# Kernel tuning notes

Hardware: AMD Instinct MI355X
Metric: run time of the kernel (lower is better)

## Reference

```python
import jax, jax.numpy as jnp
import numpy as np

# Static configuration (from init_kwargs)
SPLIT_SEC = (128, 320, 320)   # (n_nucl_species..., n_up, n_dn)
N = sum(SPLIT_SEC)            # 768 particles
N_NUCL = sum(SPLIT_SEC[:-2])  # 128
N_DN = SPLIT_SEC[-1]          # 320
SINGLE = 256
PAIR = 64
D_FEAT = SINGLE + len(SPLIT_SEC) * PAIR + len(SPLIT_SEC) * SINGLE  # 1216
SQRT2 = 1.4142135623730951
GELU_RESCALE = 1.7128586      # fvmc rescaled-gelu constant (unit output variance)

_SPLIT_IDX = np.cumsum(SPLIT_SEC)[:-1]

def _pair_type():
    pt = np.zeros((N, N), np.int32)
    sn, se = slice(0, N_NUCL), slice(N_NUCL, N)
    su = slice(N_NUCL, N_NUCL + SPLIT_SEC[-2])
    sd = slice(N_NUCL + SPLIT_SEC[-2], N)
    pt[sn, se] = pt[se, sn] = 1
    pt[su, su] = pt[sd, sd] = 2
    pt[su, sd] = pt[sd, su] = 3
    return pt

PAIR_TYPE = _pair_type()  # static int mask, values in {0,1,2,3}

def actv(x):
    # parse_activation('gelu', rescale=True)
    return jax.nn.gelu(x) * GELU_RESCALE

def residual(x, y):
    # adaptive_residual with rescale=True (shapes always match here)
    return (x + y) / SQRT2

def aggregate_features(h1, h2):
    # per-section mean of h1 over particles -> (n_sec, d1), tiled to (N, n_sec, d1)
    h1_mean = jnp.stack([s.mean(axis=0) for s in jnp.split(h1, _SPLIT_IDX, axis=0)], axis=0)
    h1_mean = jnp.tile(h1_mean[None], (N, 1, 1))
    # per-section mean of h2 over axis 1 -> (N, n_sec, d2)
    h2_mean = jnp.stack([s.mean(axis=1) for s in jnp.split(h2, _SPLIT_IDX, axis=1)], axis=-2)
    # spin symmetry: swap the last two (up/dn) mean channels for the dn rows
    h1_sw = jnp.stack([h1_mean[-N_DN:, -1], h1_mean[-N_DN:, -2]], axis=1)
    h1_mean = h1_mean.at[-N_DN:, -2:].set(h1_sw)
    h2_sw = jnp.stack([h2_mean[-N_DN:, -1], h2_mean[-N_DN:, -2]], axis=1)
    h2_mean = h2_mean.at[-N_DN:, -2:].set(h2_sw)
    return jnp.concatenate([h1, h2_mean.reshape(N, -1), h1_mean.reshape(N, -1)], axis=-1)

def setup_inputs() -> dict:
    key = jax.random.key(0)
    ks = jax.random.split(key, 5)
    sc = lambda fan_in: 1.0 / np.sqrt(fan_in)  # lecun-normal-ish scale
    return {
        "h1": jax.random.normal(ks[0], (N, SINGLE), jnp.float32),
        "h2": jax.random.normal(ks[1], (N, N, PAIR), jnp.float32),
        "W1n": jax.random.normal(ks[2], (D_FEAT, SINGLE), jnp.float32) * sc(D_FEAT),
        "b1n": jnp.zeros((SINGLE,), jnp.float32),
        "W1e": jax.random.normal(ks[3], (D_FEAT, SINGLE), jnp.float32) * sc(D_FEAT),
        "b1e": jnp.zeros((SINGLE,), jnp.float32),
        "W2": jax.random.normal(ks[4], (4, PAIR, PAIR), jnp.float32) * sc(PAIR),
        "b2": jnp.zeros((4, PAIR), jnp.float32),
    }

def reference(h1, h2, W1n, b1n, W1e, b1e, W2, b2):
    feats = aggregate_features(h1, h2)  # (N, D_FEAT)
    # h1 update: separate Dense for nuclei vs electrons
    h1_new = jnp.concatenate([
        feats[:N_NUCL] @ W1n + b1n,
        feats[N_NUCL:] @ W1e + b1e,
    ], axis=0)
    h1_out = residual(h1, actv(h1_new))
    # h2 update: per pair-type Dense, masked scatter back (4 static types)
    pt = jnp.asarray(PAIR_TYPE)
    h2_new = jnp.zeros((N, N, PAIR), h2.dtype)
    for p in range(4):
        mask = (pt == p)[..., None]
        h2_new = h2_new + mask * (jnp.einsum('nmd,de->nme', h2, W2[p]) + b2[p])
    h2_out = residual(h2, actv(h2_new))
    return h1_out, h2_out
```

## Files before the change

kernel.cpp:

```cpp
#include <hip/hip_runtime.h>


#define H1OUT_ELEMS (768 * 256)

typedef short short8 __attribute__((ext_vector_type(8)));
typedef float f32x4 __attribute__((ext_vector_type(4)));

__device__ __forceinline__ unsigned short f2bf(float f) {
    unsigned u = __builtin_bit_cast(unsigned, f);
    unsigned r = u + 0x7fffu + ((u >> 16) & 1u);
    return (unsigned short)(r >> 16);
}

__device__ __forceinline__ float bf2f(unsigned short v) {
    unsigned u = ((unsigned)v) << 16;
    return __builtin_bit_cast(float, u);
}

__device__ __forceinline__ float gelu_res(float x, float hv) {
    float x2 = x * x;
    float z = x * fmaf(-0.1029432196f, x2, -2.3025850930f);
    float e = __builtin_amdgcn_exp2f(z);
    float r = __builtin_amdgcn_rcpf(1.f + e);
    return fmaf(x * r, 1.2111740f, hv * 0.70710678f);
}

__global__ __launch_bounds__(256) void k_h2pre(
    const float* __restrict__ h2, const float* __restrict__ W2,
    const float* __restrict__ b2, const float* __restrict__ h1,
    const float* __restrict__ W1n, const float* __restrict__ W1e,
    float* __restrict__ out2, float* __restrict__ part2,
    float* __restrict__ part1, unsigned short* __restrict__ WT) {
    __shared__ union SM {
        unsigned short ot[4][16][76];
        unsigned short BT[64][72];
        float tile2[64][33];
    } sm;
    __shared__ float red[4][4][64];

    int b = blockIdx.x;
    const int t = threadIdx.x;

    if (b < 12) {
        float s = 0.f;
        #pragma unroll 8
        for (int r = 0; r < 64; ++r) s += h1[(size_t)(b * 64 + r) * 256 + t];
        part1[b * 256 + t] = s;
        return;
    }
    if (b < 316) {
        int idx = b - 12;
        int mtx = idx / 152;
        int r2  = idx % 152;
        int k0 = (r2 >> 3) * 64, e0 = (r2 & 7) * 32;
        const float* W = mtx ? W1e : W1n;
        #pragma unroll
        for (int i = 0; i < 8; ++i) {
            int j = i * 256 + t;
            int kr = j >> 5, ec = j & 31;
            sm.tile2[kr][ec] = W[(size_t)(k0 + kr) * 256 + e0 + ec];
        }
        __syncthreads();
        int er = t >> 3, k8 = (t & 7) * 8;
        short8 o;
        #pragma unroll
        for (int j = 0; j < 8; ++j) o[j] = (short)f2bf(sm.tile2[k8 + j][er]);
        *reinterpret_cast<short8*>(
            &WT[((size_t)mtx * 256 + e0 + er) * 1216 + k0 + k8]) = o;
        return;
    }

    b -= 316;
    const int ct = b % 12;
    const int n  = b / 12;
    const int m0 = ct * 64;

    const int rs = (n < 128) ? 0 : ((n < 448) ? 1 : 2);
    const int cs = (ct < 2) ? 0 : ((ct < 7) ? 1 : 2);
    int p;
    if (rs == 0)      p = (cs == 0) ? 0 : 1;
    else if (rs == 1) p = (cs == 0) ? 1 : ((cs == 1) ? 2 : 3);
    else              p = (cs == 0) ? 1 : ((cs == 1) ? 3 : 2);

    const float* src = h2 + ((size_t)n * 768 + m0) * 64;
    const int lane = t & 63;
    const int w = t >> 6;
    const int lr = lane & 15, lk = lane >> 4;
    const int r0 = w * 16;

    const float* wrow = W2 + p * 4096 + lane * 64 + w * 16;
    float4 wv4[4];
    #pragma unroll
    for (int i = 0; i < 4; ++i)
        wv4[i] = *reinterpret_cast<const float4*>(wrow + i * 4);

    const float* hbase = src + r0 * 64;
    f32x4 hv[4];
    #pragma unroll
    for (int i = 0; i < 4; ++i)
        hv[i] = *reinterpret_cast<const f32x4*>(hbase + i * 256 + lane * 4);

    const float* arow = src + (r0 + lr) * 64 + lk * 8;
    float4 af[2][2];
    #pragma unroll
    for (int kh = 0; kh < 2; ++kh) {
        af[kh][0] = *reinterpret_cast<const float4*>(arow + kh * 32);
        af[kh][1] = *reinterpret_cast<const float4*>(arow + kh * 32 + 4);
    }

    #pragma unroll
    for (int i = 0; i < 4; ++i) {
        unsigned short v0 = f2bf(wv4[i].x);
        unsigned short v1 = f2bf(wv4[i].y);
        unsigned short v2 = f2bf(wv4[i].z);
        unsigned short v3 = f2bf(wv4[i].w);
        sm.BT[w * 16 + i * 4 + 0][lane] = v0;
        sm.BT[w * 16 + i * 4 + 1][lane] = v1;
        sm.BT[w * 16 + i * 4 + 2][lane] = v2;
        sm.BT[w * 16 + i * 4 + 3][lane] = v3;
    }

    {
        f32x4 s;
        s[0] = hv[0][0] + hv[1][0] + hv[2][0] + hv[3][0];
        s[1] = hv[0][1] + hv[1][1] + hv[2][1] + hv[3][1];
        s[2] = hv[0][2] + hv[1][2] + hv[2][2] + hv[3][2];
        s[3] = hv[0][3] + hv[1][3] + hv[2][3] + hv[3][3];
        *reinterpret_cast<f32x4*>(&red[w][lane >> 4][(lane & 15) * 4]) = s;
    }

    asm volatile("s_waitcnt lgkmcnt(0)" ::: "memory");
    __builtin_amdgcn_s_barrier();
    asm volatile("" ::: "memory");

    if (t < 64) {
        float s = 0.f;
        #pragma unroll
        for (int q = 0; q < 16; ++q) s += red[q >> 2][q & 3][t];
        part2[((size_t)n * 12 + ct) * 64 + t] = s;
    }

    short8 bF[4][2];
    #pragma unroll
    for (int fe = 0; fe < 4; ++fe)
        #pragma unroll
        for (int kh = 0; kh < 2; ++kh)
            bF[fe][kh] = *reinterpret_cast<const short8*>(
                &sm.BT[fe * 16 + lr][kh * 32 + lk * 8]);

    short8 aF[2];
    #pragma unroll
    for (int kh = 0; kh < 2; ++kh) {
        short8 o;
        o[0] = (short)f2bf(af[kh][0].x);
        o[1] = (short)f2bf(af[kh][0].y);
        o[2] = (short)f2bf(af[kh][0].z);
        o[3] = (short)f2bf(af[kh][0].w);
        o[4] = (short)f2bf(af[kh][1].x);
        o[5] = (short)f2bf(af[kh][1].y);
        o[6] = (short)f2bf(af[kh][1].z);
        o[7] = (short)f2bf(af[kh][1].w);
        aF[kh] = o;
    }

    asm volatile("s_waitcnt lgkmcnt(0)" ::: "memory");
    __builtin_amdgcn_s_barrier();
    asm volatile("" ::: "memory");

    #pragma unroll
    for (int fe = 0; fe < 4; ++fe) {
        f32x4 acc = {};
        acc = __builtin_amdgcn_mfma_f32_16x16x32_bf16(aF[0], bF[fe][0], acc, 0, 0, 0);
        acc = __builtin_amdgcn_mfma_f32_16x16x32_bf16(aF[1], bF[fe][1], acc, 0, 0, 0);
        float bias = b2[p * 64 + fe * 16 + lr];
        #pragma unroll
        for (int r = 0; r < 4; ++r)
            sm.ot[w][lk * 4 + r][fe * 16 + lr] = f2bf(acc[r] + bias);
    }

    float* dst = out2 + ((size_t)n * 768 + m0 + r0) * 64;
    #pragma unroll
    for (int i = 0; i < 4; ++i) {
        int row = i * 4 + (lane >> 4), col = (lane & 15) * 4;
        ushort4 xb = *reinterpret_cast<const ushort4*>(&sm.ot[w][row][col]);
        f32x4 o;
        o[0] = gelu_res(bf2f(xb.x), hv[i][0]);
        o[1] = gelu_res(bf2f(xb.y), hv[i][1]);
        o[2] = gelu_res(bf2f(xb.z), hv[i][2]);
        o[3] = gelu_res(bf2f(xb.w), hv[i][3]);
        __builtin_nontemporal_store(
            o, reinterpret_cast<f32x4*>(dst + i * 256 + lane * 4));
    }
}

__global__ __launch_bounds__(256) void k_h1f(
    const float* __restrict__ h1, const unsigned short* __restrict__ WT,
    const float* __restrict__ part2, const float* __restrict__ part1,
    const float* __restrict__ b1n, const float* __restrict__ b1e,
    float* __restrict__ out1) {
    __shared__ unsigned short FL[16][1224];

    const int n0 = blockIdx.x * 16;
    const int half = blockIdx.y;
    const int t = threadIdx.x;
    const bool dn = (n0 >= 448);
    const bool nucl = (n0 < 128);

    #pragma unroll
    for (int i = 0; i < 16; ++i) {
        int idx = i * 256 + t;
        int r = idx >> 8, c = idx & 255;
        FL[r][c] = f2bf(h1[(size_t)(n0 + r) * 256 + c]);
    }
    #pragma unroll
    for (int i = 0; i < 12; ++i) {
        int idx = i * 256 + t;
        int r = idx / 192, c = idx % 192;
        int sec = c >> 6, d = c & 63;
        int s2 = (dn && sec >= 1) ? (3 - sec) : sec;
        const float* pr = part2 + (size_t)(n0 + r) * 768;
        float s;
        if (s2 == 0) {
            s = (pr[d] + pr[64 + d]) * (1.f / 128.f);
        } else {
            int q0 = (s2 == 1) ? 2 : 7;
            s = 0.f;
            #pragma unroll
            for (int q = 0; q < 5; ++q) s += pr[(q0 + q) * 64 + d];
            s *= (1.f / 320.f);
        }
        FL[r][256 + c] = f2bf(s);
    }
    #pragma unroll
    for (int i = 0; i < 3; ++i) {
        int j = i * 256 + t;
        int sec = j >> 8, e2 = j & 255;
        int s2 = (dn && sec >= 1) ? (3 - sec) : sec;
        float s;
        if (s2 == 0) {
            s = (part1[e2] + part1[256 + e2]) * (1.f / 128.f);
        } else {
            int q0 = (s2 == 1) ? 2 : 7;
            s = 0.f;
            #pragma unroll
            for (int q = 0; q < 5; ++q) s += part1[(q0 + q) * 256 + e2];
            s *= (1.f / 320.f);
        }
        unsigned short bv = f2bf(s);
        #pragma unroll
        for (int r = 0; r < 16; ++r) FL[r][448 + j] = bv;
    }
    __syncthreads();

    const int w = t >> 6, lane = t & 63;
    const int lr = lane & 15, lk = lane >> 4;
    const int e0 = half * 128 + w * 32;
    const unsigned short* BT = WT + (nucl ? 0 : (size_t)256 * 1216);
    const unsigned short* br0 = BT + (size_t)(e0 + lr) * 1216 + lk * 8;
    const unsigned short* br1 = br0 + (size_t)16 * 1216;
    const unsigned short* ar = &FL[lr][lk * 8];

    f32x4 acc0 = {}, acc1 = {};
    #pragma unroll 2
    for (int k = 0; k < 1216; k += 32) {
        short8 aF = *reinterpret_cast<const short8*>(ar + k);
        short8 b0 = *reinterpret_cast<const short8*>(br0 + k);
        short8 b1 = *reinterpret_cast<const short8*>(br1 + k);
        acc0 = __builtin_amdgcn_mfma_f32_16x16x32_bf16(b0, aF, acc0, 0, 0, 0);
        acc1 = __builtin_amdgcn_mfma_f32_16x16x32_bf16(b1, aF, acc1, 0, 0, 0);
    }

    const float* bb = nucl ? b1n : b1e;
    const int m = n0 + lr;
    #pragma unroll
    for (int j = 0; j < 2; ++j) {
        const f32x4 a = j ? acc1 : acc0;
        int e = e0 + j * 16 + lk * 4;
        f32x4 bias4 = *reinterpret_cast<const f32x4*>(bb + e);
        f32x4 hv = *reinterpret_cast<const f32x4*>(h1 + (size_t)m * 256 + e);
        f32x4 o;
        o[0] = gelu_res(a[0] + bias4[0], hv[0]);
        o[1] = gelu_res(a[1] + bias4[1], hv[1]);
        o[2] = gelu_res(a[2] + bias4[2], hv[2]);
        o[3] = gelu_res(a[3] + bias4[3], hv[3]);
        *reinterpret_cast<f32x4*>(out1 + (size_t)m * 256 + e) = o;
    }
}

extern "C" void kernel_launch(void* const* d_in, const int* in_sizes, int n_in,
                              void* d_out, int out_size, void* d_ws, size_t ws_size,
                              hipStream_t stream) {
    const float* h1  = (const float*)d_in[0];
    const float* h2  = (const float*)d_in[1];
    const float* W1n = (const float*)d_in[2];
    const float* b1n = (const float*)d_in[3];
    const float* W1e = (const float*)d_in[4];
    const float* b1e = (const float*)d_in[5];
    const float* W2  = (const float*)d_in[6];
    const float* b2  = (const float*)d_in[7];

    float* out1 = (float*)d_out;
    float* out2 = out1 + H1OUT_ELEMS;

    float* part2 = (float*)d_ws;
    float* part1 = part2 + 768 * 12 * 64;
    unsigned short* WT = (unsigned short*)(part1 + 12 * 256);

    k_h2pre<<<dim3(316 + 12 * 768), 256, 0, stream>>>(
        h2, W2, b2, h1, W1n, W1e, out2, part2, part1, WT);
    k_h1f<<<dim3(48, 2), 256, 0, stream>>>(h1, WT, part2, part1, b1n, b1e, out1);
}
```

Measured before the change: 73.25 us.

## Remove block barriers in h2 kernel via direct W2 fragment loads and shuffle reductions

Each wave now loads its bf16 W2 MFMA fragments straight from global memory with strided scalar reads, instead of staging them transposed through shared memory. The partial column sums for the h2 means are reduced with cross-lane shuffles and written per wave as bf16, with no shared-memory reduction. This removes both block-wide barriers and the LDS traffic in the 9216-block main kernel. In exchange it issues more uncoalesced global loads for W2, quadruples the number of partial entries the h1 kernel must sum, and rounds the partial sums to bf16 before they are averaged.

Measured after the change: 80.91 us. 1.1x slower.

```diff
diff --git a/kernel.cpp b/kernel.cpp
--- a/kernel.cpp
+++ b/kernel.cpp
@@ -29,14 +29,12 @@
     const float* __restrict__ h2, const float* __restrict__ W2,
     const float* __restrict__ b2, const float* __restrict__ h1,
     const float* __restrict__ W1n, const float* __restrict__ W1e,
-    float* __restrict__ out2, float* __restrict__ part2,
+    float* __restrict__ out2, unsigned short* __restrict__ part2b,
     float* __restrict__ part1, unsigned short* __restrict__ WT) {
     __shared__ union SM {
         unsigned short ot[4][16][76];
-        unsigned short BT[64][72];
         float tile2[64][33];
     } sm;
-    __shared__ float red[4][4][64];
 
     int b = blockIdx.x;
     const int t = threadIdx.x;
@@ -88,11 +86,20 @@
     const int lr = lane & 15, lk = lane >> 4;
     const int r0 = w * 16;
 
-    const float* wrow = W2 + p * 4096 + lane * 64 + w * 16;
-    float4 wv4[4];
-    #pragma unroll
-    for (int i = 0; i < 4; ++i)
-        wv4[i] = *reinterpret_cast<const float4*>(wrow + i * 4);
+    const float* wp = W2 + p * 4096;
+    short8 bF[4][2];
+    #pragma unroll
+    for (int fe = 0; fe < 4; ++fe) {
+        const float* q = wp + fe * 16 + lr;
+        #pragma unroll
+        for (int kh = 0; kh < 2; ++kh) {
+            short8 o;
+            #pragma unroll
+            for (int j = 0; j < 8; ++j)
+                o[j] = (short)f2bf(q[(kh * 32 + lk * 8 + j) * 64]);
+            bF[fe][kh] = o;
+        }
+    }
 
     const float* hbase = src + r0 * 64;
     f32x4 hv[4];
@@ -106,18 +113,6 @@
     for (int kh = 0; kh < 2; ++kh) {
         af[kh][0] = *reinterpret_cast<const float4*>(arow + kh * 32);
         af[kh][1] = *reinterpret_cast<const float4*>(arow + kh * 32 + 4);
-    }
-
-    #pragma unroll
-    for (int i = 0; i < 4; ++i) {
-        unsigned short v0 = f2bf(wv4[i].x);
-        unsigned short v1 = f2bf(wv4[i].y);
-        unsigned short v2 = f2bf(wv4[i].z);
-        unsigned short v3 = f2bf(wv4[i].w);
-        sm.BT[w * 16 + i * 4 + 0][lane] = v0;
-        sm.BT[w * 16 + i * 4 + 1][lane] = v1;
-        sm.BT[w * 16 + i * 4 + 2][lane] = v2;
-        sm.BT[w * 16 + i * 4 + 3][lane] = v3;
     }
 
     {
@@ -126,27 +121,20 @@
         s[1] = hv[0][1] + hv[1][1] + hv[2][1] + hv[3][1];
         s[2] = hv[0][2] + hv[1][2] + hv[2][2] + hv[3][2];
         s[3] = hv[0][3] + hv[1][3] + hv[2][3] + hv[3][3];
-        *reinterpret_cast<f32x4*>(&red[w][lane >> 4][(lane & 15) * 4]) = s;
-    }
-
-    asm volatile("s_waitcnt lgkmcnt(0)" ::: "memory");
-    __builtin_amdgcn_s_barrier();
-    asm volatile("" ::: "memory");
-
-    if (t < 64) {
-        float s = 0.f;
-        #pragma unroll
-        for (int q = 0; q < 16; ++q) s += red[q >> 2][q & 3][t];
-        part2[((size_t)n * 12 + ct) * 64 + t] = s;
-    }
-
-    short8 bF[4][2];
-    #pragma unroll
-    for (int fe = 0; fe < 4; ++fe)
-        #pragma unroll
-        for (int kh = 0; kh < 2; ++kh)
-            bF[fe][kh] = *reinterpret_cast<const short8*>(
-                &sm.BT[fe * 16 + lr][kh * 32 + lk * 8]);
+        #pragma unroll
+        for (int k = 0; k < 4; ++k) {
+            s[k] += __shfl_xor(s[k], 16);
+            s[k] += __shfl_xor(s[k], 32);
+        }
+        if (lane < 16) {
+            unsigned short* pb =
+                part2b + ((size_t)(n * 12 + ct) * 64 + lane * 4) * 4 + w;
+            pb[0]  = f2bf(s[0]);
+            pb[4]  = f2bf(s[1]);
+            pb[8]  = f2bf(s[2]);
+            pb[12] = f2bf(s[3]);
+        }
+    }
 
     short8 aF[2];
     #pragma unroll
@@ -163,10 +151,6 @@
         aF[kh] = o;
     }
 
-    asm volatile("s_waitcnt lgkmcnt(0)" ::: "memory");
-    __builtin_amdgcn_s_barrier();
-    asm volatile("" ::: "memory");
-
     #pragma unroll
     for (int fe = 0; fe < 4; ++fe) {
         f32x4 acc = {};
@@ -195,7 +179,7 @@
 
 __global__ __launch_bounds__(256) void k_h1f(
     const float* __restrict__ h1, const unsigned short* __restrict__ WT,
-    const float* __restrict__ part2, const float* __restrict__ part1,
+    const unsigned short* __restrict__ part2b, const float* __restrict__ part1,
     const float* __restrict__ b1n, const float* __restrict__ b1e,
     float* __restrict__ out1) {
     __shared__ unsigned short FL[16][1224];
@@ -218,15 +202,24 @@
         int r = idx / 192, c = idx % 192;
         int sec = c >> 6, d = c & 63;
         int s2 = (dn && sec >= 1) ? (3 - sec) : sec;
-        const float* pr = part2 + (size_t)(n0 + r) * 768;
-        float s;
+        const unsigned short* pr = part2b + (size_t)(n0 + r) * 3072;
+        float s = 0.f;
         if (s2 == 0) {
-            s = (pr[d] + pr[64 + d]) * (1.f / 128.f);
+            #pragma unroll
+            for (int q = 0; q < 2; ++q) {
+                ushort4 v = *reinterpret_cast<const ushort4*>(
+                    pr + ((size_t)q * 64 + d) * 4);
+                s += bf2f(v.x) + bf2f(v.y) + bf2f(v.z) + bf2f(v.w);
+            }
+            s *= (1.f / 128.f);
         } else {
             int q0 = (s2 == 1) ? 2 : 7;
-            s = 0.f;
             #pragma unroll
-            for (int q = 0; q < 5; ++q) s += pr[(q0 + q) * 64 + d];
+            for (int q = 0; q < 5; ++q) {
+                ushort4 v = *reinterpret_cast<const ushort4*>(
+                    pr + ((size_t)(q0 + q) * 64 + d) * 4);
+                s += bf2f(v.x) + bf2f(v.y) + bf2f(v.z) + bf2f(v.w);
+            }
             s *= (1.f / 320.f);
         }
         FL[r][256 + c] = f2bf(s);
@@ -302,11 +295,11 @@
     float* out1 = (float*)d_out;
     float* out2 = out1 + H1OUT_ELEMS;
 
-    float* part2 = (float*)d_ws;
-    float* part1 = part2 + 768 * 12 * 64;
+    unsigned short* part2b = (unsigned short*)d_ws;
+    float* part1 = (float*)(part2b + (size_t)768 * 3072);
     unsigned short* WT = (unsigned short*)(part1 + 12 * 256);
 
     k_h2pre<<<dim3(316 + 12 * 768), 256, 0, stream>>>(
-        h2, W2, b2, h1, W1n, W1e, out2, part2, part1, WT);
-    k_h1f<<<dim3(48, 2), 256, 0, stream>>>(h1, WT, part2, part1, b1n, b1e, out1);
-}
+        h2, W2, b2, h1, W1n, W1e, out2, part2b, part1, WT);
+    k_h1f<<<dim3(48, 2), 256, 0, stream>>>(h1, WT, part2b, part1, b1n, b1e, out1);
+}
```
